# Performance work log

Hardware: AMD Instinct MI355X
Metric: run time of the kernel (lower is better)

Reference implementation:

```python
import jax, jax.numpy as jnp
import numpy as np

H1, W1GRID, K_SIZE, B = 28, 28, 5, 512
K2 = K_SIZE * K_SIZE  # 25 kernel weight matrices
_BITS = np.array([[0, 0], [0, 1], [1, 0], [1, 1]])  # 2^dim basis combos


def _grid_edges(h, w):
    """8-neighborhood grid graph; returns (src, dst, pseudo in [0,1]^2)."""
    ys, xs = np.meshgrid(np.arange(h), np.arange(w), indexing='ij')
    node = (ys * w + xs).reshape(-1)
    ys, xs = ys.reshape(-1), xs.reshape(-1)
    srcs, dsts, pses = [], [], []
    for dy in (-1, 0, 1):
        for dx in (-1, 0, 1):
            if dy == 0 and dx == 0:
                continue
            ny, nx = ys + dy, xs + dx
            ok = (ny >= 0) & (ny < h) & (nx >= 0) & (nx < w)
            srcs.append((ny * w + nx)[ok])   # neighbor j
            dsts.append(node[ok])            # center i
            p = np.array([[(dx + 1) / 2.0, (dy + 1) / 2.0]], dtype=np.float32)
            pses.append(np.repeat(p, ok.sum(), axis=0))
    return (np.concatenate(srcs), np.concatenate(dsts), np.concatenate(pses))


def _batched_graph(h, w, batch):
    s, d, p = _grid_edges(h, w)
    n = h * w
    off = (np.arange(batch, dtype=np.int64) * n)[:, None]
    src = (s[None, :] + off).reshape(-1)
    dst = (d[None, :] + off).reshape(-1)
    pse = np.tile(p, (batch, 1))
    return np.stack([src, dst]), pse


def setup_inputs() -> dict:
    key = jax.random.key(0)
    ks = jax.random.split(key, 8)
    e1, p1 = _batched_graph(28, 28, B)
    e2, p2 = _batched_graph(14, 14, B)
    return {
        'x': jax.random.uniform(ks[0], (B * 784, 1), jnp.float32),
        'pseudo1': jnp.asarray(p1), 'pseudo2': jnp.asarray(p2),
        'W1': jax.random.normal(ks[1], (K2, 1, 32), jnp.float32) * 0.2,
        'root1': jax.random.normal(ks[2], (1, 32), jnp.float32) * 0.2,
        'b1': jnp.zeros((32,), jnp.float32),
        'W2': jax.random.normal(ks[3], (K2, 32, 64), jnp.float32) * 0.05,
        'root2': jax.random.normal(ks[4], (32, 64), jnp.float32) * 0.05,
        'b2': jnp.zeros((64,), jnp.float32),
        'fc1_w': jax.random.normal(ks[5], (3136, 512), jnp.float32) * 0.02,
        'fc1_b': jnp.zeros((512,), jnp.float32),
        'fc2_w': jax.random.normal(ks[6], (512, 10), jnp.float32) * 0.05,
        'fc2_b': jnp.zeros((10,), jnp.float32),
        'edge_index1': jnp.asarray(e1, jnp.int64 if jax.config.jax_enable_x64 else jnp.int32),
        'edge_index2': jnp.asarray(e2, jnp.int64 if jax.config.jax_enable_x64 else jnp.int32),
    }


def _spline_basis(pseudo, k):
    # open B-spline, degree 1: each dim contributes 2 knots with linear weights
    frac = pseudo * (k - 1)                                   # [E,2]
    lo = jnp.clip(jnp.floor(frac), 0, k - 2)
    f = frac - lo                                             # [E,2]
    w = jnp.stack([1.0 - f, f], axis=-1)                      # [E,2,2]
    idx = jnp.stack([lo, lo + 1], axis=-1).astype(jnp.int32)  # [E,2,2]
    basis = w[:, 0, _BITS[:, 0]] * w[:, 1, _BITS[:, 1]]       # [E,4]
    widx = idx[:, 0, _BITS[:, 0]] + idx[:, 1, _BITS[:, 1]] * k  # [E,4]
    return basis, widx


def _spline_conv(x, edge_index, pseudo, W, root, bias, n_nodes, k):
    src, dst = edge_index[0], edge_index[1]
    x_j = x[src]                                              # [E,Cin] gather
    basis, widx = _spline_basis(pseudo, k)                    # [E,4]
    kk = k * k
    flat = (dst[:, None] * kk + widx).reshape(-1)             # [E*4]
    contrib = (basis[:, :, None] * x_j[:, None, :]).reshape(-1, x.shape[1])
    S = jnp.zeros((n_nodes * kk, x.shape[1]), x.dtype).at[flat].add(contrib)
    S = S.reshape(n_nodes, kk, x.shape[1])                    # per-node per-kernel sums
    deg = jnp.zeros((n_nodes,), x.dtype).at[dst].add(1.0)
    out = jnp.einsum('nki,kio->no', S, W) / jnp.maximum(deg, 1.0)[:, None]
    return out + x @ root + bias


def _pool2x2(x, b, hw, c):
    return x.reshape(b, hw // 2, 2, hw // 2, 2, c).max(axis=(2, 4))


def reference(x, pseudo1, pseudo2, W1, root1, b1, W2, root2, b2,
              fc1_w, fc1_b, fc2_w, fc2_b, edge_index1, edge_index2):
    n1 = x.shape[0]
    b = n1 // 784
    h = jax.nn.elu(_spline_conv(x, edge_index1, pseudo1, W1, root1, b1, n1, K_SIZE))
    h = _pool2x2(h, b, 28, 32).reshape(-1, 32)                # [B*196,32]
    h = jax.nn.elu(_spline_conv(h, edge_index2, pseudo2, W2, root2, b2, b * 196, K_SIZE))
    h = _pool2x2(h, b, 14, 64).reshape(-1, 7 * 7 * 64)        # [B,3136]
    h = jax.nn.elu(h @ fc1_w + fc1_b)
    # dropout is identity in eval mode
    h = jax.nn.elu(h @ fc2_w + fc2_b)
    return jax.nn.log_softmax(h, axis=-1)
```

## Files before the change

### kernel.cpp

```cpp
#include <hip/hip_runtime.h>
#include <math.h>

#define BATCH 512

typedef float v2f __attribute__((ext_vector_type(2)));

__device__ __forceinline__ float elu1(float v) {
    return v > 0.f ? v : expm1f(v);
}

__global__ __launch_bounds__(256) void k12_conv12(
    const float* __restrict__ x, const float* __restrict__ W1,
    const float* __restrict__ root1, const float* __restrict__ b1,
    const float* __restrict__ W2, const float* __restrict__ root2,
    const float* __restrict__ b2, float* __restrict__ p2) {
    __shared__ float xs1[900];
    __shared__ float w1s[320];
    __shared__ float xs2[8192];
    __shared__ float wb[2304];
    const int b = blockIdx.x;
    const int t = threadIdx.x;

    static const int widx_t[8] = {0, 2, 4, 10, 14, 20, 22, 24};
    static const int ddy[8] = {-1,-1,-1, 0, 0, 1, 1, 1};
    static const int ddx[8] = {-1, 0, 1,-1, 1,-1, 0, 1};

    for (int l = t; l < 900; l += 256) xs1[l] = 0.f;
    {
        int d = t >> 5, c = t & 31;
        int e = d + (d >= 4 ? 1 : 0);
        int dy = e / 3 - 1, dx = e % 3 - 1;
        int widx = 2 * (dx + 1) + 10 * (dy + 1);
        w1s[t] = W1[widx * 32 + c];
        if (t < 32) { w1s[256 + t] = root1[t]; w1s[288 + t] = b1[t]; }
    }
    {
        const float4* s4 = (const float4*)W2;
        float4 v0 = s4[t], v1 = s4[t + 256];
        *(float4*)(wb + (t >> 4) * 72 + (t & 15) * 4) = v0;
        *(float4*)(wb + ((t + 256) >> 4) * 72 + (t & 15) * 4) = v1;
    }
    {
        float4 z = make_float4(0.f, 0.f, 0.f, 0.f);
        float4* x4 = (float4*)xs2;
        for (int l = t; l < 480; l += 256) {
            int nd = l >> 3, B = l & 7;
            int y, xx;
            if (nd < 16)      { y = 0;       xx = nd; }
            else if (nd < 32) { y = 15;      xx = nd - 16; }
            else if (nd < 46) { y = nd - 31; xx = 0; }
            else              { y = nd - 45; xx = 15; }
            x4[B * 256 + y * 16 + xx] = z;
        }
    }
    __syncthreads();
    {
        const float* xb = x + (size_t)b * 784;
        for (int l = t; l < 784; l += 256) {
            int y = l / 28, xx = l % 28;
            xs1[(y + 1) * 30 + xx + 1] = xb[l];
        }
    }
    __syncthreads();

    if (t < 196) {
        int py = t / 14, px = t % 14;
        int xbse[4];
        float xc[4], inv1[4];
        #pragma unroll
        for (int p = 0; p < 4; ++p) {
            int sy = p >> 1, sx = p & 1;
            int y = 2 * py + sy, xx = 2 * px + sx;
            xbse[p] = (y + 1) * 30 + xx + 1;
            xc[p] = xs1[xbse[p]];
            int nvy = 3 - (y == 0) - (y == 27);
            int nvx = 3 - (xx == 0) - (xx == 27);
            inv1[p] = 1.f / (float)(nvy * nvx - 1);
        }
        const float4* w4 = (const float4*)w1s;
        const int npw = (py + 1) * 16 + px + 1;
        float4* out4 = (float4*)xs2;

        #pragma unroll
        for (int h = 0; h < 2; ++h) {
            float4 acc[4][4];
            #pragma unroll
            for (int p = 0; p < 4; ++p)
                #pragma unroll
                for (int q = 0; q < 4; ++q) acc[p][q] = make_float4(0.f, 0.f, 0.f, 0.f);
            #pragma unroll
            for (int d = 0; d < 8; ++d) {
                int e = d + (d >= 4 ? 1 : 0);
                int od = (e / 3 - 1) * 30 + (e % 3 - 1);
                float4 w0 = w4[d * 8 + h * 4 + 0];
                float4 w1 = w4[d * 8 + h * 4 + 1];
                float4 w2 = w4[d * 8 + h * 4 + 2];
                float4 w3 = w4[d * 8 + h * 4 + 3];
                #pragma unroll
                for (int p = 0; p < 4; ++p) {
                    float xv = xs1[xbse[p] + od];
                    acc[p][0].x += xv * w0.x; acc[p][0].y += xv * w0.y; acc[p][0].z += xv * w0.z; acc[p][0].w += xv * w0.w;
                    acc[p][1].x += xv * w1.x; acc[p][1].y += xv * w1.y; acc[p][1].z += xv * w1.z; acc[p][1].w += xv * w1.w;
                    acc[p][2].x += xv * w2.x; acc[p][2].y += xv * w2.y; acc[p][2].z += xv * w2.z; acc[p][2].w += xv * w2.w;
                    acc[p][3].x += xv * w3.x; acc[p][3].y += xv * w3.y; acc[p][3].z += xv * w3.z; acc[p][3].w += xv * w3.w;
                }
            }
            #pragma unroll
            for (int q = 0; q < 4; ++q) {
                float4 rt = w4[64 + h * 4 + q];
                float4 bs = w4[72 + h * 4 + q];
                float4 m = make_float4(-1e30f, -1e30f, -1e30f, -1e30f);
                #pragma unroll
                for (int p = 0; p < 4; ++p) {
                    float4 v;
                    v.x = elu1(acc[p][q].x * inv1[p] + xc[p] * rt.x + bs.x);
                    v.y = elu1(acc[p][q].y * inv1[p] + xc[p] * rt.y + bs.y);
                    v.z = elu1(acc[p][q].z * inv1[p] + xc[p] * rt.z + bs.z);
                    v.w = elu1(acc[p][q].w * inv1[p] + xc[p] * rt.w + bs.w);
                    m.x = fmaxf(m.x, v.x); m.y = fmaxf(m.y, v.y);
                    m.z = fmaxf(m.z, v.z); m.w = fmaxf(m.w, v.w);
                }
                out4[(h * 4 + q) * 256 + npw] = m;
            }
        }
    }
    __syncthreads();

    int tile = t >> 3; if (tile > 27) tile = 27;
    const int cg = t & 7;
    const int py2 = tile >> 2, q2 = tile & 3;
    int npb[8]; float invd[8];
    #pragma unroll
    for (int p = 0; p < 8; ++p) {
        int r = p >> 2, c = p & 3;
        int gy = 2 * py2 + r, gx = 4 * q2 + c;
        npb[p] = (gy + 1) * 16 + gx + 1;
        int gxc = gx > 13 ? 13 : gx;
        int nvy = 3 - (gy == 0) - (gy == 13);
        int nvx = 3 - (gxc == 0) - (gxc == 13);
        invd[p] = 1.f / (float)(nvy * nvx - 1);
    }

    v2f acc2[8][4];
    #pragma unroll
    for (int p = 0; p < 8; ++p)
        #pragma unroll
        for (int j = 0; j < 4; ++j) acc2[p][j] = (v2f){0.f, 0.f};

    const float4* xs4 = (const float4*)xs2;
    for (int d = 0; d < 9; ++d) {
        float4 pf0, pf1;
        if (d < 8) {
            const float* nsrc = (d + 1 == 8) ? root2 : (W2 + (size_t)widx_t[d + 1] * 2048);
            pf0 = ((const float4*)nsrc)[t];
            pf1 = ((const float4*)nsrc)[t + 256];
        }
        if (d == 8) {
            #pragma unroll
            for (int p = 0; p < 8; ++p) {
                v2f iv = {invd[p], invd[p]};
                #pragma unroll
                for (int j = 0; j < 4; ++j) acc2[p][j] *= iv;
            }
        }
        int dnode = (d < 8) ? (ddy[d] * 16 + ddx[d]) : 0;
        const float4* xp[8];
        #pragma unroll
        for (int p = 0; p < 8; ++p) xp[p] = xs4 + (npb[p] + dnode);

        #pragma unroll 2
        for (int i4 = 0; i4 < 8; ++i4) {
            float xa[8][4];
            #pragma unroll
            for (int p = 0; p < 8; ++p) {
                float4 v = xp[p][i4 * 256];
                xa[p][0] = v.x; xa[p][1] = v.y; xa[p][2] = v.z; xa[p][3] = v.w;
            }
            #pragma unroll
            for (int ii = 0; ii < 4; ++ii) {
                const float* wr = wb + (i4 * 4 + ii) * 72 + cg * 8;
                float4 w0 = *(const float4*)wr;
                float4 w1 = *(const float4*)(wr + 4);
                v2f w2v[4] = {{w0.x, w0.y}, {w0.z, w0.w}, {w1.x, w1.y}, {w1.z, w1.w}};
                #pragma unroll
                for (int p = 0; p < 8; ++p) {
                    v2f xv2 = {xa[p][ii], xa[p][ii]};
                    acc2[p][0] += xv2 * w2v[0];
                    acc2[p][1] += xv2 * w2v[1];
                    acc2[p][2] += xv2 * w2v[2];
                    acc2[p][3] += xv2 * w2v[3];
                }
            }
        }
        if (d < 8) {
            __syncthreads();
            *(float4*)(wb + (t >> 4) * 72 + (t & 15) * 4) = pf0;
            *(float4*)(wb + ((t + 256) >> 4) * 72 + (t & 15) * 4) = pf1;
            __syncthreads();
        }
    }

    if (t < 224) {
        float4 bs0 = *(const float4*)(b2 + cg * 8);
        float4 bs1 = *(const float4*)(b2 + cg * 8 + 4);
        float bsv[8] = {bs0.x, bs0.y, bs0.z, bs0.w, bs1.x, bs1.y, bs1.z, bs1.w};
        float* outb = p2 + (size_t)b * 3136;
        #pragma unroll
        for (int cc = 0; cc < 2; ++cc) {
            int cellcol = 2 * q2 + cc;
            if (cellcol > 6) continue;
            float mv[8];
            #pragma unroll
            for (int j = 0; j < 8; ++j) mv[j] = -1e30f;
            #pragma unroll
            for (int r = 0; r < 2; ++r)
            #pragma unroll
            for (int c2 = 0; c2 < 2; ++c2) {
                int p = r * 4 + cc * 2 + c2;
                #pragma unroll
                for (int j = 0; j < 8; ++j) {
                    float v = elu1(acc2[p][j >> 1][j & 1] + bsv[j]);
                    mv[j] = fmaxf(mv[j], v);
                }
            }
            int cell = py2 * 7 + cellcol;
            *(float4*)(outb + cell * 64 + cg * 8)     = make_float4(mv[0], mv[1], mv[2], mv[3]);
            *(float4*)(outb + cell * 64 + cg * 8 + 4) = make_float4(mv[4], mv[5], mv[6], mv[7]);
        }
    }
}

__global__ __launch_bounds__(256) void k3a_fc1(
    const float* __restrict__ A, const float* __restrict__ B,
    float* __restrict__ part) {
    __shared__ float As[2][16][64];
    __shared__ float Bs[2][16][72];
    const int t = threadIdx.x;
    const int tx = t & 15, ty = t >> 4;
    const int n0 = blockIdx.x * 64, m0 = blockIdx.y * 64;
    const int k0 = blockIdx.z * 272;
    const int steps = ((blockIdx.z == 11) ? 144 : 272) >> 4;

    const int sm = t & 63, k4 = t >> 6;
    const int sk = t >> 4, sc = t & 15;
    const float* Ap = A + (size_t)(m0 + sm) * 3136 + k0 + k4 * 4;
    const float* Bp = B + (size_t)(k0 + sk) * 512 + n0 + sc * 4;

    {
        float4 av = *(const float4*)Ap;
        float4 bv = *(const float4*)Bp;
        As[0][k4 * 4 + 0][sm] = av.x; As[0][k4 * 4 + 1][sm] = av.y;
        As[0][k4 * 4 + 2][sm] = av.z; As[0][k4 * 4 + 3][sm] = av.w;
        *(float4*)&Bs[0][sk][sc * 4] = bv;
    }
    __syncthreads();

    float acc[4][4];
    #pragma unroll
    for (int r = 0; r < 4; ++r)
        #pragma unroll
        for (int c = 0; c < 4; ++c) acc[r][c] = 0.f;

    for (int s = 0; s < steps; ++s) {
        float4 a0, b0;
        if (s + 1 < steps) {
            a0 = *(const float4*)(Ap + (s + 1) * 16);
            b0 = *(const float4*)(Bp + (size_t)(s + 1) * 16 * 512);
        }
        const int cur = s & 1;
        #pragma unroll
        for (int k = 0; k < 16; ++k) {
            float4 a4 = *(const float4*)&As[cur][k][ty * 4];
            float4 b4 = *(const float4*)&Bs[cur][k][tx * 4];
            acc[0][0] += a4.x * b4.x; acc[0][1] += a4.x * b4.y; acc[0][2] += a4.x * b4.z; acc[0][3] += a4.x * b4.w;
            acc[1][0] += a4.y * b4.x; acc[1][1] += a4.y * b4.y; acc[1][2] += a4.y * b4.z; acc[1][3] += a4.y * b4.w;
            acc[2][0] += a4.z * b4.x; acc[2][1] += a4.z * b4.y; acc[2][2] += a4.z * b4.z; acc[2][3] += a4.z * b4.w;
            acc[3][0] += a4.w * b4.x; acc[3][1] += a4.w * b4.y; acc[3][2] += a4.w * b4.z; acc[3][3] += a4.w * b4.w;
        }
        if (s + 1 < steps) {
            const int nxt = cur ^ 1;
            As[nxt][k4 * 4 + 0][sm] = a0.x; As[nxt][k4 * 4 + 1][sm] = a0.y;
            As[nxt][k4 * 4 + 2][sm] = a0.z; As[nxt][k4 * 4 + 3][sm] = a0.w;
            *(float4*)&Bs[nxt][sk][sc * 4] = b0;
        }
        __syncthreads();
    }

    float* pbase = part + ((size_t)blockIdx.z * 512 + m0 + ty * 4) * 512 + n0;
    #pragma unroll
    for (int r = 0; r < 4; ++r)
        *(float4*)(pbase + (size_t)r * 512 + tx * 4) =
            make_float4(acc[r][0], acc[r][1], acc[r][2], acc[r][3]);
}

__global__ __launch_bounds__(256) void k34_reduce_fc2_lsm(
    const float* __restrict__ part, const float* __restrict__ fc1b,
    const float* __restrict__ w, const float* __restrict__ fc2b,
    float* __restrict__ out, int KZ) {
    __shared__ float red[4][10];
    const int b = blockIdx.x, t = threadIdx.x;

    float a0 = fc1b[t], a1 = fc1b[t + 256];
    for (int kz = 0; kz < KZ; ++kz) {
        const float* pr = part + ((size_t)kz * 512 + b) * 512;
        a0 += pr[t]; a1 += pr[t + 256];
    }
    a0 = elu1(a0); a1 = elu1(a1);

    float acc[10];
    #pragma unroll
    for (int o = 0; o < 10; ++o)
        acc[o] = a0 * w[t * 10 + o] + a1 * w[(t + 256) * 10 + o];
    #pragma unroll
    for (int s = 32; s; s >>= 1)
        #pragma unroll
        for (int o = 0; o < 10; ++o) acc[o] += __shfl_xor(acc[o], s, 64);
    if ((t & 63) == 0) {
        #pragma unroll
        for (int o = 0; o < 10; ++o) red[t >> 6][o] = acc[o];
    }
    __syncthreads();
    if (t == 0) {
        float v[10], m = -1e30f;
        #pragma unroll
        for (int o = 0; o < 10; ++o) {
            float s = red[0][o] + red[1][o] + red[2][o] + red[3][o] + fc2b[o];
            v[o] = elu1(s);
            m = fmaxf(m, v[o]);
        }
        float ssum = 0.f;
        #pragma unroll
        for (int o = 0; o < 10; ++o) ssum += expf(v[o] - m);
        float lse = m + logf(ssum);
        #pragma unroll
        for (int o = 0; o < 10; ++o) out[(size_t)b * 10 + o] = v[o] - lse;
    }
}

extern "C" void kernel_launch(void* const* d_in, const int* in_sizes, int n_in,
                              void* d_out, int out_size, void* d_ws, size_t ws_size,
                              hipStream_t stream) {
    const float* x     = (const float*)d_in[0];
    const float* W1    = (const float*)d_in[3];
    const float* root1 = (const float*)d_in[4];
    const float* b1v   = (const float*)d_in[5];
    const float* W2    = (const float*)d_in[6];
    const float* root2 = (const float*)d_in[7];
    const float* b2v   = (const float*)d_in[8];
    const float* fc1w  = (const float*)d_in[9];
    const float* fc1b  = (const float*)d_in[10];
    const float* fc2w  = (const float*)d_in[11];
    const float* fc2b  = (const float*)d_in[12];

    float* ws = (float*)d_ws;
    float* part = ws;
    float* p2 = ws + 3211264;

    k12_conv12<<<dim3(BATCH), 256, 0, stream>>>(x, W1, root1, b1v, W2, root2, b2v, p2);
    k3a_fc1<<<dim3(8, 8, 12), 256, 0, stream>>>(p2, fc1w, part);
    k34_reduce_fc2_lsm<<<dim3(BATCH), 256, 0, stream>>>(part, fc1b, fc2w, fc2b, (float*)d_out, 12);
}
```

Before: 118.0 us.

## Enlarge fc1 GEMM tiles to 128x128 and register-prefetch conv2 inputs

The fc1 GEMM tile grows from 64x64 to 128x128 per block, with 8x8 outputs per thread and wider vector loads. This raises arithmetic intensity and cuts shared-memory traffic per FMA, but the grid shrinks to 192 blocks, which may underfill the GPU's compute units and adds register pressure. The conv2 inner loop is also restructured to double-buffer the float4 input loads in registers and to use explicit packed vector FMAs, so LDS reads can overlap with math.

```diff
diff --git a/kernel.cpp b/kernel.cpp
--- a/kernel.cpp
+++ b/kernel.cpp
@@ -5,8 +5,38 @@
 
 typedef float v2f __attribute__((ext_vector_type(2)));
 
+#if __has_builtin(__builtin_elementwise_fma)
+#define VFMA(a, b, c) __builtin_elementwise_fma(a, b, c)
+#else
+static __device__ __forceinline__ v2f vfma_(v2f a, v2f b, v2f c) {
+    v2f r; r.x = fmaf(a.x, b.x, c.x); r.y = fmaf(a.y, b.y, c.y); return r;
+}
+#define VFMA(a, b, c) vfma_(a, b, c)
+#endif
+
 __device__ __forceinline__ float elu1(float v) {
     return v > 0.f ? v : expm1f(v);
+}
+
+__device__ __forceinline__ void conv2_step(const float* __restrict__ wb, int cg, int I4,
+                                           const float4* XB, v2f acc2[8][4]) {
+    #pragma unroll
+    for (int ii = 0; ii < 4; ++ii) {
+        const float* wr = wb + (I4 * 4 + ii) * 72 + cg * 8;
+        float4 w0 = *(const float4*)wr;
+        float4 w1 = *(const float4*)(wr + 4);
+        v2f wv0 = {w0.x, w0.y}, wv1 = {w0.z, w0.w};
+        v2f wv2 = {w1.x, w1.y}, wv3 = {w1.z, w1.w};
+        #pragma unroll
+        for (int p = 0; p < 8; ++p) {
+            float xsv = (ii == 0) ? XB[p].x : (ii == 1) ? XB[p].y : (ii == 2) ? XB[p].z : XB[p].w;
+            v2f xv2 = {xsv, xsv};
+            acc2[p][0] = VFMA(xv2, wv0, acc2[p][0]);
+            acc2[p][1] = VFMA(xv2, wv1, acc2[p][1]);
+            acc2[p][2] = VFMA(xv2, wv2, acc2[p][2]);
+            acc2[p][3] = VFMA(xv2, wv3, acc2[p][3]);
+        }
+    }
 }
 
 __global__ __launch_bounds__(256) void k12_conv12(
@@ -168,30 +198,21 @@
         #pragma unroll
         for (int p = 0; p < 8; ++p) xp[p] = xs4 + (npb[p] + dnode);
 
-        #pragma unroll 2
-        for (int i4 = 0; i4 < 8; ++i4) {
-            float xa[8][4];
-            #pragma unroll
-            for (int p = 0; p < 8; ++p) {
-                float4 v = xp[p][i4 * 256];
-                xa[p][0] = v.x; xa[p][1] = v.y; xa[p][2] = v.z; xa[p][3] = v.w;
-            }
-            #pragma unroll
-            for (int ii = 0; ii < 4; ++ii) {
-                const float* wr = wb + (i4 * 4 + ii) * 72 + cg * 8;
-                float4 w0 = *(const float4*)wr;
-                float4 w1 = *(const float4*)(wr + 4);
-                v2f w2v[4] = {{w0.x, w0.y}, {w0.z, w0.w}, {w1.x, w1.y}, {w1.z, w1.w}};
-                #pragma unroll
-                for (int p = 0; p < 8; ++p) {
-                    v2f xv2 = {xa[p][ii], xa[p][ii]};
-                    acc2[p][0] += xv2 * w2v[0];
-                    acc2[p][1] += xv2 * w2v[1];
-                    acc2[p][2] += xv2 * w2v[2];
-                    acc2[p][3] += xv2 * w2v[3];
-                }
-            }
-        }
+        float4 xc_[8], xn_[8];
+        #pragma unroll
+        for (int p = 0; p < 8; ++p) xc_[p] = xp[p][0];
+        #pragma unroll
+        for (int i4 = 0; i4 < 8; i4 += 2) {
+            #pragma unroll
+            for (int p = 0; p < 8; ++p) xn_[p] = xp[p][(i4 + 1) * 256];
+            conv2_step(wb, cg, i4, xc_, acc2);
+            if (i4 < 6) {
+                #pragma unroll
+                for (int p = 0; p < 8; ++p) xc_[p] = xp[p][(i4 + 2) * 256];
+            }
+            conv2_step(wb, cg, i4 + 1, xn_, acc2);
+        }
+
         if (d < 8) {
             __syncthreads();
             *(float4*)(wb + (t >> 4) * 72 + (t & 15) * 4) = pf0;
@@ -233,64 +254,83 @@
 __global__ __launch_bounds__(256) void k3a_fc1(
     const float* __restrict__ A, const float* __restrict__ B,
     float* __restrict__ part) {
-    __shared__ float As[2][16][64];
-    __shared__ float Bs[2][16][72];
+    __shared__ float As[2][16][128];
+    __shared__ float Bs[2][16][132];
     const int t = threadIdx.x;
     const int tx = t & 15, ty = t >> 4;
-    const int n0 = blockIdx.x * 64, m0 = blockIdx.y * 64;
+    const int n0 = blockIdx.x * 128, m0 = blockIdx.y * 128;
     const int k0 = blockIdx.z * 272;
     const int steps = ((blockIdx.z == 11) ? 144 : 272) >> 4;
 
-    const int sm = t & 63, k4 = t >> 6;
-    const int sk = t >> 4, sc = t & 15;
-    const float* Ap = A + (size_t)(m0 + sm) * 3136 + k0 + k4 * 4;
-    const float* Bp = B + (size_t)(k0 + sk) * 512 + n0 + sc * 4;
+    const int sm = t & 127, skh = t >> 7;
+    const int sk = t >> 4, snq = t & 15;
+    const float* Ap = A + (size_t)(m0 + sm) * 3136 + k0 + skh * 8;
+    const float* Bp = B + (size_t)(k0 + sk) * 512 + n0 + snq * 8;
 
     {
-        float4 av = *(const float4*)Ap;
-        float4 bv = *(const float4*)Bp;
-        As[0][k4 * 4 + 0][sm] = av.x; As[0][k4 * 4 + 1][sm] = av.y;
-        As[0][k4 * 4 + 2][sm] = av.z; As[0][k4 * 4 + 3][sm] = av.w;
-        *(float4*)&Bs[0][sk][sc * 4] = bv;
+        float4 a0 = *(const float4*)Ap;
+        float4 a1 = *(const float4*)(Ap + 4);
+        float4 b0 = *(const float4*)Bp;
+        float4 b1 = *(const float4*)(Bp + 4);
+        As[0][skh * 8 + 0][sm] = a0.x; As[0][skh * 8 + 1][sm] = a0.y;
+        As[0][skh * 8 + 2][sm] = a0.z; As[0][skh * 8 + 3][sm] = a0.w;
+        As[0][skh * 8 + 4][sm] = a1.x; As[0][skh * 8 + 5][sm] = a1.y;
+        As[0][skh * 8 + 6][sm] = a1.z; As[0][skh * 8 + 7][sm] = a1.w;
+        *(float4*)&Bs[0][sk][snq * 8] = b0;
+        *(float4*)&Bs[0][sk][snq * 8 + 4] = b1;
     }
     __syncthreads();
 
-    float acc[4][4];
-    #pragma unroll
-    for (int r = 0; r < 4; ++r)
-        #pragma unroll
-        for (int c = 0; c < 4; ++c) acc[r][c] = 0.f;
+    float acc[8][8];
+    #pragma unroll
+    for (int r = 0; r < 8; ++r)
+        #pragma unroll
+        for (int c = 0; c < 8; ++c) acc[r][c] = 0.f;
 
     for (int s = 0; s < steps; ++s) {
-        float4 a0, b0;
+        float4 a0, a1, b0, b1;
         if (s + 1 < steps) {
             a0 = *(const float4*)(Ap + (s + 1) * 16);
+            a1 = *(const float4*)(Ap + (s + 1) * 16 + 4);
             b0 = *(const float4*)(Bp + (size_t)(s + 1) * 16 * 512);
+            b1 = *(const float4*)(Bp + (size_t)(s + 1) * 16 * 512 + 4);
         }
         const int cur = s & 1;
         #pragma unroll
         for (int k = 0; k < 16; ++k) {
-            float4 a4 = *(const float4*)&As[cur][k][ty * 4];
-            float4 b4 = *(const float4*)&Bs[cur][k][tx * 4];
-            acc[0][0] += a4.x * b4.x; acc[0][1] += a4.x * b4.y; acc[0][2] += a4.x * b4.z; acc[0][3] += a4.x * b4.w;
-            acc[1][0] += a4.y * b4.x; acc[1][1] += a4.y * b4.y; acc[1][2] += a4.y * b4.z; acc[1][3] += a4.y * b4.w;
-            acc[2][0] += a4.z * b4.x; acc[2][1] += a4.z * b4.y; acc[2][2] += a4.z * b4.z; acc[2][3] += a4.z * b4.w;
-            acc[3][0] += a4.w * b4.x; acc[3][1] += a4.w * b4.y; acc[3][2] += a4.w * b4.z; acc[3][3] += a4.w * b4.w;
+            float4 av0 = *(const float4*)&As[cur][k][ty * 8];
+            float4 av1 = *(const float4*)&As[cur][k][ty * 8 + 4];
+            float4 bv0 = *(const float4*)&Bs[cur][k][tx * 4];
+            float4 bv1 = *(const float4*)&Bs[cur][k][64 + tx * 4];
+            float ar[8] = {av0.x, av0.y, av0.z, av0.w, av1.x, av1.y, av1.z, av1.w};
+            #pragma unroll
+            for (int r = 0; r < 8; ++r) {
+                acc[r][0] += ar[r] * bv0.x; acc[r][1] += ar[r] * bv0.y;
+                acc[r][2] += ar[r] * bv0.z; acc[r][3] += ar[r] * bv0.w;
+                acc[r][4] += ar[r] * bv1.x; acc[r][5] += ar[r] * bv1.y;
+                acc[r][6] += ar[r] * bv1.z; acc[r][7] += ar[r] * bv1.w;
+            }
         }
         if (s + 1 < steps) {
             const int nxt = cur ^ 1;
-            As[nxt][k4 * 4 + 0][sm] = a0.x; As[nxt][k4 * 4 + 1][sm] = a0.y;
-            As[nxt][k4 * 4 + 2][sm] = a0.z; As[nxt][k4 * 4 + 3][sm] = a0.w;
-            *(float4*)&Bs[nxt][sk][sc * 4] = b0;
+            As[nxt][skh * 8 + 0][sm] = a0.x; As[nxt][skh * 8 + 1][sm] = a0.y;
+            As[nxt][skh * 8 + 2][sm] = a0.z; As[nxt][skh * 8 + 3][sm] = a0.w;
+            As[nxt][skh * 8 + 4][sm] = a1.x; As[nxt][skh * 8 + 5][sm] = a1.y;
+            As[nxt][skh * 8 + 6][sm] = a1.z; As[nxt][skh * 8 + 7][sm] = a1.w;
+            *(float4*)&Bs[nxt][sk][snq * 8] = b0;
+            *(float4*)&Bs[nxt][sk][snq * 8 + 4] = b1;
         }
         __syncthreads();
     }
 
-    float* pbase = part + ((size_t)blockIdx.z * 512 + m0 + ty * 4) * 512 + n0;
-    #pragma unroll
-    for (int r = 0; r < 4; ++r)
-        *(float4*)(pbase + (size_t)r * 512 + tx * 4) =
-            make_float4(acc[r][0], acc[r][1], acc[r][2], acc[r][3]);
+    float* pbase = part + ((size_t)blockIdx.z * 512 + m0 + ty * 8) * 512 + n0;
+    #pragma unroll
+    for (int r = 0; r < 8; ++r) {
+        float4 o0 = make_float4(acc[r][0], acc[r][1], acc[r][2], acc[r][3]);
+        float4 o1 = make_float4(acc[r][4], acc[r][5], acc[r][6], acc[r][7]);
+        *(float4*)(pbase + (size_t)r * 512 + tx * 4) = o0;
+        *(float4*)(pbase + (size_t)r * 512 + 64 + tx * 4) = o1;
+    }
 }
 
 __global__ __launch_bounds__(256) void k34_reduce_fc2_lsm(
@@ -357,6 +397,6 @@
     float* p2 = ws + 3211264;
 
     k12_conv12<<<dim3(BATCH), 256, 0, stream>>>(x, W1, root1, b1v, W2, root2, b2v, p2);
-    k3a_fc1<<<dim3(8, 8, 12), 256, 0, stream>>>(p2, fc1w, part);
+    k3a_fc1<<<dim3(4, 4, 12), 256, 0, stream>>>(p2, fc1w, part);
     k34_reduce_fc2_lsm<<<dim3(BATCH), 256, 0, stream>>>(part, fc1b, fc2w, fc2b, (float*)d_out, 12);
 }
```

Measured after the change: 229.3 us. +94.3%, slower.
